# Kernel optimization log

Measured on AMD Instinct MI355X. Metric: run time of the kernel, lower is better.

The kernel has to match this reference:

```python
import jax, jax.numpy as jnp
import numpy as np

LATENT = 128
HIDDEN = 512
N_STEPS = 50
BATCH = 8192


def _linear_init(k, fan_in, fan_out):
    kw, kb = jax.random.split(k)
    lim = 1.0 / np.sqrt(fan_in)
    W = jax.random.uniform(kw, (fan_in, fan_out), minval=-lim, maxval=lim, dtype=jnp.float32)
    b = jax.random.uniform(kb, (fan_out,), minval=-lim, maxval=lim, dtype=jnp.float32)
    return W, b


def setup_inputs() -> dict:
    key = jax.random.key(0)
    ks = jax.random.split(key, 6)
    in_dim = 2 * LATENT + 2  # x + condition + t_emb + target_emb
    W1, b1 = _linear_init(ks[0], in_dim, HIDDEN)
    W2, b2 = _linear_init(ks[1], HIDDEN, HIDDEN)
    W3, b3 = _linear_init(ks[2], HIDDEN, HIDDEN)
    W4, b4 = _linear_init(ks[3], HIDDEN, LATENT)
    condition = jax.random.normal(ks[4], (BATCH, LATENT), dtype=jnp.float32)
    x_init = jax.random.normal(ks[5], (BATCH, LATENT), dtype=jnp.float32)
    return dict(condition=condition, x_init=x_init,
                W1=W1, b1=b1, W2=W2, b2=b2, W3=W3, b3=b3, W4=W4, b4=b4,
                target_survival=1)


def reference(condition, x_init, W1, b1, W2, b2, W3, b3, W4, b4, target_survival):
    n_steps = N_STEPS
    betas = jnp.linspace(1e-4, 0.02, n_steps).astype(x_init.dtype)
    alphas = 1.0 - betas
    alphas_cumprod = jnp.cumprod(alphas)
    batch = condition.shape[0]
    # target = zeros if target_survival else ones (static python scalar)
    target = jnp.full((batch, 1), 0.0 if target_survival else 1.0, dtype=x_init.dtype)
    noise_key = jax.random.key(42)

    def step(x, t):
        t_emb = jnp.full((batch, 1), 1.0, x.dtype) * (t.astype(x.dtype) / n_steps)
        inp = jnp.concatenate([x, condition, t_emb, target], axis=-1)  # [B, 2L+2]
        h = jax.nn.gelu(inp @ W1 + b1, approximate=False)
        h = jax.nn.gelu(h @ W2 + b2, approximate=False)
        h = jax.nn.gelu(h @ W3 + b3, approximate=False)
        noise_pred = h @ W4 + b4  # [B, L]
        noise = jax.random.normal(jax.random.fold_in(noise_key, t), x.shape, x.dtype)
        noise = jnp.where(t > 0, noise, jnp.zeros_like(noise))  # no noise at t=0
        beta_t = betas[t]
        x = (x - beta_t / jnp.sqrt(1.0 - alphas_cumprod[t]) * noise_pred) / jnp.sqrt(alphas[t])
        x = x + jnp.sqrt(beta_t) * noise
        return x, None

    ts = jnp.arange(n_steps - 1, -1, -1)  # reversed(range(n_steps))
    x_final, _ = jax.lax.scan(step, x_init, ts)
    return x_final
```

## Files before the change

### kernel.cpp

```cpp
#include <hip/hip_runtime.h>
#include <stdint.h>
#include <stddef.h>


typedef __bf16 bf16;
typedef __bf16 bf16x4 __attribute__((ext_vector_type(4)));
typedef __bf16 bf16x8 __attribute__((ext_vector_type(8)));
typedef float  floatx4 __attribute__((ext_vector_type(4)));

#define NSTEPS    50
#define WG_ROWS   32
#define XB_STRIDE 136
#define H_STRIDE  520

__device__ __forceinline__ uint32_t rotl32(uint32_t x, int r) {
  return (x << r) | (x >> (32 - r));
}

__device__ __forceinline__ void threefry2x32(uint32_t k0, uint32_t k1,
                                             uint32_t x0, uint32_t x1,
                                             uint32_t& o0, uint32_t& o1) {
  uint32_t k2 = k0 ^ k1 ^ 0x1BD11BDAu;
  x0 += k0; x1 += k1;
#define TF_R(R) { x0 += x1; x1 = rotl32(x1, R); x1 ^= x0; }
  TF_R(13) TF_R(15) TF_R(26) TF_R(6)
  x0 += k1; x1 += k2 + 1u;
  TF_R(17) TF_R(29) TF_R(16) TF_R(24)
  x0 += k2; x1 += k0 + 2u;
  TF_R(13) TF_R(15) TF_R(26) TF_R(6)
  x0 += k0; x1 += k1 + 3u;
  TF_R(17) TF_R(29) TF_R(16) TF_R(24)
  x0 += k1; x1 += k2 + 4u;
  TF_R(13) TF_R(15) TF_R(26) TF_R(6)
  x0 += k2; x1 += k0 + 5u;
#undef TF_R
  o0 = x0; o1 = x1;
}

__device__ __forceinline__ float erfinv_xla(float x) {
  float w = -0.6931471805599453f * __builtin_amdgcn_logf(fmaf(-x, x, 1.0f));
  float p;
  if (w < 5.0f) {
    w -= 2.5f;
    p = 2.81022636e-08f;
    p = fmaf(p, w, 3.43273939e-07f);
    p = fmaf(p, w, -3.5233877e-06f);
    p = fmaf(p, w, -4.39150654e-06f);
    p = fmaf(p, w, 0.00021858087f);
    p = fmaf(p, w, -0.00125372503f);
    p = fmaf(p, w, -0.00417768164f);
    p = fmaf(p, w, 0.246640727f);
    p = fmaf(p, w, 1.50140941f);
  } else {
    w = __builtin_amdgcn_sqrtf(w) - 3.0f;
    p = -0.000200214257f;
    p = fmaf(p, w, 0.000100950558f);
    p = fmaf(p, w, 0.00134934322f);
    p = fmaf(p, w, -0.00367342844f);
    p = fmaf(p, w, 0.00573950773f);
    p = fmaf(p, w, -0.0076224613f);
    p = fmaf(p, w, 0.00943887047f);
    p = fmaf(p, w, 1.00167406f);
    p = fmaf(p, w, 2.83297682f);
  }
  return p * x;
}

__device__ __forceinline__ float gelu_fast(float x) {
  float z  = x * 0.7071067811865475f;
  float az = fabsf(z);
  float t  = __builtin_amdgcn_rcpf(fmaf(0.3275911f, az, 1.0f));
  float p  = fmaf(1.061405429f, t, -1.453152027f);
  p = fmaf(p, t, 1.421413741f);
  p = fmaf(p, t, -0.284496736f);
  p = fmaf(p, t, 0.254829592f);
  p *= t;
  float e  = __builtin_amdgcn_exp2f(az * az * -1.4426950408889634f);
  float er = fmaf(-p, e, 1.0f);
  er = copysignf(er, z);
  return 0.5f * x * (1.0f + er);
}

template<int KSTEPS, int BSTRIDE, int UNROLL>
__device__ __forceinline__ void gemm2t(const bf16* __restrict__ h_lds,
                                       const bf16* __restrict__ A_pk,
                                       int lane, floatx4 (&acc)[2][2]) {
  const int nrow = lane & 15, q = lane >> 4;
  const bf16* b0 = h_lds + nrow * BSTRIDE + q * 8;
  const bf16* a0 = A_pk + lane * 8;
#pragma unroll UNROLL
  for (int ks = 0; ks < KSTEPS; ++ks) {
    bf16x8 bf0 = *(const bf16x8*)(b0 + ks * 32);
    bf16x8 bf1 = *(const bf16x8*)(b0 + 16 * BSTRIDE + ks * 32);
    bf16x8 aA  = *(const bf16x8*)(a0 + ks * 512);
    bf16x8 aB  = *(const bf16x8*)(a0 + (KSTEPS + ks) * 512);
    acc[0][0] = __builtin_amdgcn_mfma_f32_16x16x32_bf16(aA, bf0, acc[0][0], 0, 0, 0);
    acc[0][1] = __builtin_amdgcn_mfma_f32_16x16x32_bf16(aA, bf1, acc[0][1], 0, 0, 0);
    acc[1][0] = __builtin_amdgcn_mfma_f32_16x16x32_bf16(aB, bf0, acc[1][0], 0, 0, 0);
    acc[1][1] = __builtin_amdgcn_mfma_f32_16x16x32_bf16(aB, bf1, acc[1][1], 0, 0, 0);
  }
}

template<int KSTEPS, int BSTRIDE>
__device__ __forceinline__ void gemm1t(const bf16* __restrict__ h_lds,
                                       const bf16* __restrict__ A_pk,
                                       int lane, floatx4& acc) {
  const int nrow = lane & 15, q = lane >> 4;
  const bf16* b0 = h_lds + nrow * BSTRIDE + q * 8;
  const bf16* a0 = A_pk + lane * 8;
#pragma unroll 4
  for (int ks = 0; ks < KSTEPS; ++ks) {
    bf16x8 bfr = *(const bf16x8*)(b0 + ks * 32);
    bf16x8 af  = *(const bf16x8*)(a0 + ks * 512);
    acc = __builtin_amdgcn_mfma_f32_16x16x32_bf16(af, bfr, acc, 0, 0, 0);
  }
}

__global__ void diff_prep(const float* __restrict__ W1, const float* __restrict__ b1,
                          const float* __restrict__ W2, const float* __restrict__ W3,
                          const float* __restrict__ W4, const int* __restrict__ tsurv,
                          bf16* __restrict__ w1p, bf16* __restrict__ w1cp,
                          bf16* __restrict__ w2p, bf16* __restrict__ w3p,
                          bf16* __restrict__ w4p,
                          float* __restrict__ eb1, uint32_t* __restrict__ fk,
                          float* __restrict__ cst) {
  const int tid = blockIdx.x * blockDim.x + threadIdx.x;
  const int nth = gridDim.x * blockDim.x;
  for (int i = tid; i < 512 * 128; i += nth) {
    int j = i & 7, lane = (i >> 3) & 63, ks = (i >> 9) & 3, ntg = i >> 11;
    int n = ntg * 16 + (lane & 15);
    int k = ks * 32 + (lane >> 4) * 8 + j;
    w1p[i]  = (bf16)W1[k * 512 + n];
    w1cp[i] = (bf16)W1[(128 + k) * 512 + n];
  }
  for (int i = tid; i < 512 * 512; i += nth) {
    int j = i & 7, lane = (i >> 3) & 63, ks = (i >> 9) & 15, ntg = i >> 13;
    int n = ntg * 16 + (lane & 15);
    int k = ks * 32 + (lane >> 4) * 8 + j;
    w2p[i] = (bf16)W2[k * 512 + n];
    w3p[i] = (bf16)W3[k * 512 + n];
  }
  for (int i = tid; i < 128 * 512; i += nth) {
    int j = i & 7, lane = (i >> 3) & 63, ks = (i >> 9) & 15, ntg = i >> 13;
    int n = ntg * 16 + (lane & 15);
    int k = ks * 32 + (lane >> 4) * 8 + j;
    w4p[i] = (bf16)W4[k * 128 + n];
  }
  const float tgt = (tsurv[0] != 0) ? 0.0f : 1.0f;
  for (int i = tid; i < NSTEPS * 512; i += nth) {
    int t = i >> 9, n = i & 511;
    eb1[i] = b1[n] + ((float)t / 50.0f) * W1[256 * 512 + n] + tgt * W1[257 * 512 + n];
  }
  if (tid == 0) {
    float ac = 1.0f;
    for (int t = 0; t < NSTEPS; ++t) {
      float beta  = 1e-4f + (0.02f - 1e-4f) * ((float)t / 49.0f);
      float alpha = 1.0f - beta;
      ac *= alpha;
      cst[t]            = beta / sqrtf(1.0f - ac);
      cst[NSTEPS + t]   = 1.0f / sqrtf(alpha);
      cst[2*NSTEPS + t] = sqrtf(beta);
      uint32_t o0, o1;
      threefry2x32(0u, 42u, 0u, (uint32_t)t, o0, o1);
      fk[t] = o0; fk[NSTEPS + t] = o1;
    }
  }
}

__global__ __launch_bounds__(1024, 4) void diff_main(
    const float* __restrict__ cond, const float* __restrict__ xinit,
    const bf16* __restrict__ w1p, const bf16* __restrict__ w1cp,
    const bf16* __restrict__ w2p, const bf16* __restrict__ w3p,
    const bf16* __restrict__ w4p,
    const float* __restrict__ eb1, const float* __restrict__ b2,
    const float* __restrict__ b3, const float* __restrict__ b4,
    const uint32_t* __restrict__ fk, const float* __restrict__ cst,
    float* __restrict__ out) {
  __shared__ bf16 xb[WG_ROWS * XB_STRIDE];
  __shared__ bf16 hbA[WG_ROWS * H_STRIDE];
  __shared__ bf16 hbB[WG_ROWS * H_STRIDE];

  const int tid  = threadIdx.x;
  const int wave = tid >> 6;
  const int lane = tid & 63;
  const int nrow = lane & 15, q = lane >> 4;
  const int r0   = blockIdx.x * WG_ROWS;
  const int mc0  = wave * 32;
  const int qc   = q * 4;

  const int mtile4 = wave & 7;
  const int ntile4 = wave >> 3;
  const int n4     = ntile4 * 16 + nrow;
  const int xc0    = mtile4 * 16 + qc;

  {
    const int row = tid >> 5;
    const int c4  = (tid & 31) * 4;
    float4 a = *(const float4*)(xinit + (size_t)(r0 + row) * 128 + c4);
    float4 c = *(const float4*)(cond  + (size_t)(r0 + row) * 128 + c4);
    bf16x4 x4, c4v;
    x4[0] = (bf16)a.x; x4[1] = (bf16)a.y; x4[2] = (bf16)a.z; x4[3] = (bf16)a.w;
    c4v[0] = (bf16)c.x; c4v[1] = (bf16)c.y; c4v[2] = (bf16)c.z; c4v[3] = (bf16)c.w;
    *(bf16x4*)(xb  + row * XB_STRIDE + c4) = x4;
    *(bf16x4*)(hbA + row * H_STRIDE  + c4) = c4v;
  }
  float4 xreg = *(const float4*)(xinit + (size_t)(r0 + n4) * 128 + xc0);
  __syncthreads();

  floatx4 cpr[2][2] = {};
  gemm2t<4, H_STRIDE, 4>(hbA, w1cp + (wave * 2) * 4 * 512, lane, cpr);
  __syncthreads();

  for (int t = NSTEPS - 1; t >= 0; --t) {
    {
      floatx4 acc[2][2] = {};
      gemm2t<4, XB_STRIDE, 4>(xb, w1p + (wave * 2) * 4 * 512, lane, acc);
      const float* ebt = eb1 + t * 512;
#pragma unroll
      for (int mt = 0; mt < 2; ++mt) {
        const int col = mc0 + mt * 16 + qc;
        float4 bb = *(const float4*)(ebt + col);
#pragma unroll
        for (int nt = 0; nt < 2; ++nt) {
          bf16x4 g;
#pragma unroll
          for (int r = 0; r < 4; ++r)
            g[r] = (bf16)gelu_fast(acc[mt][nt][r] + cpr[mt][nt][r] + ((const float*)&bb)[r]);
          *(bf16x4*)(hbA + (nt * 16 + nrow) * H_STRIDE + col) = g;
        }
      }
    }
    __syncthreads();

    {
      floatx4 acc[2][2] = {};
      gemm2t<16, H_STRIDE, 4>(hbA, w2p + (wave * 2) * 16 * 512, lane, acc);
#pragma unroll
      for (int mt = 0; mt < 2; ++mt) {
        const int col = mc0 + mt * 16 + qc;
        float4 bb = *(const float4*)(b2 + col);
#pragma unroll
        for (int nt = 0; nt < 2; ++nt) {
          bf16x4 g;
#pragma unroll
          for (int r = 0; r < 4; ++r)
            g[r] = (bf16)gelu_fast(acc[mt][nt][r] + ((const float*)&bb)[r]);
          *(bf16x4*)(hbB + (nt * 16 + nrow) * H_STRIDE + col) = g;
        }
      }
    }
    __syncthreads();

    {
      floatx4 acc[2][2] = {};
      gemm2t<16, H_STRIDE, 4>(hbB, w3p + (wave * 2) * 16 * 512, lane, acc);
#pragma unroll
      for (int mt = 0; mt < 2; ++mt) {
        const int col = mc0 + mt * 16 + qc;
        float4 bb = *(const float4*)(b3 + col);
#pragma unroll
        for (int nt = 0; nt < 2; ++nt) {
          bf16x4 g;
#pragma unroll
          for (int r = 0; r < 4; ++r)
            g[r] = (bf16)gelu_fast(acc[mt][nt][r] + ((const float*)&bb)[r]);
          *(bf16x4*)(hbA + (nt * 16 + nrow) * H_STRIDE + col) = g;
        }
      }
    }
    __syncthreads();

    {
      floatx4 acc = {};
      gemm1t<16, H_STRIDE>(hbA + ntile4 * 16 * H_STRIDE,
                           w4p + mtile4 * 16 * 512, lane, acc);
      const float c1 = cst[t], c2 = cst[NSTEPS + t], c3 = cst[2 * NSTEPS + t];
      const uint32_t fk0 = fk[t], fk1 = fk[NSTEPS + t];
      float4 bb = *(const float4*)(b4 + xc0);
      const uint32_t gbase = (uint32_t)(r0 + n4) * 128u + (uint32_t)xc0;
      bf16x4 xpk;
#pragma unroll
      for (int r = 0; r < 4; ++r) {
        float np = acc[r] + ((const float*)&bb)[r];
        float z = 0.0f;
        if (t > 0) {
          uint32_t o0, o1;
          threefry2x32(fk0, fk1, 0u, gbase + (uint32_t)r, o0, o1);
          uint32_t bits = o0 ^ o1;
          float f01 = __uint_as_float((bits >> 9) | 0x3F800000u) - 1.0f;
          float u = f01 * 2.0f + (-0.99999994f);
          u = fmaxf(-0.99999994f, u);
          z = 1.4142135381698608f * erfinv_xla(u);
        }
        float xn = (((float*)&xreg)[r] - c1 * np) * c2 + c3 * z;
        ((float*)&xreg)[r] = xn;
        xpk[r] = (bf16)xn;
      }
      *(bf16x4*)(xb + n4 * XB_STRIDE + xc0) = xpk;
    }
    __syncthreads();
  }

  *(float4*)(out + (size_t)(r0 + n4) * 128 + xc0) = xreg;
}

extern "C" void kernel_launch(void* const* d_in, const int* in_sizes, int n_in,
                              void* d_out, int out_size, void* d_ws, size_t ws_size,
                              hipStream_t stream) {
  const float* cond  = (const float*)d_in[0];
  const float* xinit = (const float*)d_in[1];
  const float* W1 = (const float*)d_in[2];
  const float* b1 = (const float*)d_in[3];
  const float* W2 = (const float*)d_in[4];
  const float* b2 = (const float*)d_in[5];
  const float* W3 = (const float*)d_in[6];
  const float* b3 = (const float*)d_in[7];
  const float* W4 = (const float*)d_in[8];
  const float* b4 = (const float*)d_in[9];
  const int* tsurv = (const int*)d_in[10];

  char* ws = (char*)d_ws;
  bf16* w1p  = (bf16*)(ws + 0);
  bf16* w1cp = (bf16*)(ws + 131072);
  bf16* w2p  = (bf16*)(ws + 262144);
  bf16* w3p  = (bf16*)(ws + 786432);
  bf16* w4p  = (bf16*)(ws + 1310720);
  float* eb1 = (float*)(ws + 1441792);
  uint32_t* fkp = (uint32_t*)(ws + 1544192);
  float* cstp = (float*)(ws + 1544704);

  diff_prep<<<1024, 256, 0, stream>>>(W1, b1, W2, W3, W4, tsurv,
                                      w1p, w1cp, w2p, w3p, w4p, eb1, fkp, cstp);
  diff_main<<<256, 1024, 0, stream>>>(cond, xinit, w1p, w1cp, w2p, w3p, w4p,
                                      eb1, b2, b3, b4, fkp, cstp, (float*)d_out);
}
```

Measured before the change: 995.2 us.

## Keep W1 in registers, prefetch next-layer weights, use lighter barriers

Caches the per-wave W1 fragments in registers for all timesteps, so they are no longer reloaded from global memory at each step. It prefetches the first two k-steps of W2, W3 and W4 fragments before the preceding barrier and epilogue to hide global load latency. It also replaces __syncthreads with an inline s_waitcnt lgkmcnt(0) plus s_barrier, and uses alignbit for the rotates. The extra live registers may reduce occupancy. The custom barrier relies on LDS traffic being the only dependency that needs ordering.

Result: slower. 2.149 ms (+115.9%).

```diff
diff --git a/kernel.cpp b/kernel.cpp
--- a/kernel.cpp
+++ b/kernel.cpp
@@ -13,8 +13,10 @@
 #define XB_STRIDE 136
 #define H_STRIDE  520
 
+#define BAR_LGKM() asm volatile("s_waitcnt lgkmcnt(0)\n\ts_barrier" ::: "memory")
+
 __device__ __forceinline__ uint32_t rotl32(uint32_t x, int r) {
-  return (x << r) | (x >> (32 - r));
+  return __builtin_amdgcn_alignbit(x, x, 32u - (uint32_t)r);
 }
 
 __device__ __forceinline__ void threefry2x32(uint32_t k0, uint32_t k1,
@@ -102,14 +104,54 @@
 }
 
 template<int KSTEPS, int BSTRIDE>
-__device__ __forceinline__ void gemm1t(const bf16* __restrict__ h_lds,
-                                       const bf16* __restrict__ A_pk,
-                                       int lane, floatx4& acc) {
+__device__ __forceinline__ void gemm2t_pre(const bf16* __restrict__ h_lds,
+                                           const bf16* __restrict__ A_pk,
+                                           int lane,
+                                           bf16x8 pA0, bf16x8 pA1,
+                                           bf16x8 pB0, bf16x8 pB1,
+                                           floatx4 (&acc)[2][2]) {
   const int nrow = lane & 15, q = lane >> 4;
   const bf16* b0 = h_lds + nrow * BSTRIDE + q * 8;
   const bf16* a0 = A_pk + lane * 8;
+  {
+    bf16x8 bf0 = *(const bf16x8*)(b0);
+    bf16x8 bf1 = *(const bf16x8*)(b0 + 16 * BSTRIDE);
+    acc[0][0] = __builtin_amdgcn_mfma_f32_16x16x32_bf16(pA0, bf0, acc[0][0], 0, 0, 0);
+    acc[0][1] = __builtin_amdgcn_mfma_f32_16x16x32_bf16(pA0, bf1, acc[0][1], 0, 0, 0);
+    acc[1][0] = __builtin_amdgcn_mfma_f32_16x16x32_bf16(pB0, bf0, acc[1][0], 0, 0, 0);
+    acc[1][1] = __builtin_amdgcn_mfma_f32_16x16x32_bf16(pB0, bf1, acc[1][1], 0, 0, 0);
+    bf0 = *(const bf16x8*)(b0 + 32);
+    bf1 = *(const bf16x8*)(b0 + 16 * BSTRIDE + 32);
+    acc[0][0] = __builtin_amdgcn_mfma_f32_16x16x32_bf16(pA1, bf0, acc[0][0], 0, 0, 0);
+    acc[0][1] = __builtin_amdgcn_mfma_f32_16x16x32_bf16(pA1, bf1, acc[0][1], 0, 0, 0);
+    acc[1][0] = __builtin_amdgcn_mfma_f32_16x16x32_bf16(pB1, bf0, acc[1][0], 0, 0, 0);
+    acc[1][1] = __builtin_amdgcn_mfma_f32_16x16x32_bf16(pB1, bf1, acc[1][1], 0, 0, 0);
+  }
 #pragma unroll 4
-  for (int ks = 0; ks < KSTEPS; ++ks) {
+  for (int ks = 2; ks < KSTEPS; ++ks) {
+    bf16x8 bf0 = *(const bf16x8*)(b0 + ks * 32);
+    bf16x8 bf1 = *(const bf16x8*)(b0 + 16 * BSTRIDE + ks * 32);
+    bf16x8 aA  = *(const bf16x8*)(a0 + ks * 512);
+    bf16x8 aB  = *(const bf16x8*)(a0 + (KSTEPS + ks) * 512);
+    acc[0][0] = __builtin_amdgcn_mfma_f32_16x16x32_bf16(aA, bf0, acc[0][0], 0, 0, 0);
+    acc[0][1] = __builtin_amdgcn_mfma_f32_16x16x32_bf16(aA, bf1, acc[0][1], 0, 0, 0);
+    acc[1][0] = __builtin_amdgcn_mfma_f32_16x16x32_bf16(aB, bf0, acc[1][0], 0, 0, 0);
+    acc[1][1] = __builtin_amdgcn_mfma_f32_16x16x32_bf16(aB, bf1, acc[1][1], 0, 0, 0);
+  }
+}
+
+template<int KSTEPS, int BSTRIDE>
+__device__ __forceinline__ void gemm1t_pre(const bf16* __restrict__ h_lds,
+                                           const bf16* __restrict__ A_pk,
+                                           int lane, bf16x8 p0, bf16x8 p1,
+                                           floatx4& acc) {
+  const int nrow = lane & 15, q = lane >> 4;
+  const bf16* b0 = h_lds + nrow * BSTRIDE + q * 8;
+  const bf16* a0 = A_pk + lane * 8;
+  acc = __builtin_amdgcn_mfma_f32_16x16x32_bf16(p0, *(const bf16x8*)(b0), acc, 0, 0, 0);
+  acc = __builtin_amdgcn_mfma_f32_16x16x32_bf16(p1, *(const bf16x8*)(b0 + 32), acc, 0, 0, 0);
+#pragma unroll 4
+  for (int ks = 2; ks < KSTEPS; ++ks) {
     bf16x8 bfr = *(const bf16x8*)(b0 + ks * 32);
     bf16x8 af  = *(const bf16x8*)(a0 + ks * 512);
     acc = __builtin_amdgcn_mfma_f32_16x16x32_bf16(af, bfr, acc, 0, 0, 0);
@@ -193,6 +235,11 @@
   const int n4     = ntile4 * 16 + nrow;
   const int xc0    = mtile4 * 16 + qc;
 
+  const bf16* w1a = w1p + (wave * 2) * 4 * 512 + lane * 8;
+  const bf16* w2a = w2p + (wave * 2) * 16 * 512 + lane * 8;
+  const bf16* w3a = w3p + (wave * 2) * 16 * 512 + lane * 8;
+  const bf16* w4a = w4p + mtile4 * 16 * 512 + lane * 8;
+
   {
     const int row = tid >> 5;
     const int c4  = (tid & 31) * 4;
@@ -205,16 +252,39 @@
     *(bf16x4*)(hbA + row * H_STRIDE  + c4) = c4v;
   }
   float4 xreg = *(const float4*)(xinit + (size_t)(r0 + n4) * 128 + xc0);
+  const uint32_t gbase = (uint32_t)(r0 + n4) * 128u + (uint32_t)xc0;
+
+  bf16x8 w1r[2][4];
+#pragma unroll
+  for (int mt = 0; mt < 2; ++mt)
+#pragma unroll
+    for (int ks = 0; ks < 4; ++ks)
+      w1r[mt][ks] = *(const bf16x8*)(w1a + (mt * 4 + ks) * 512);
+
   __syncthreads();
 
   floatx4 cpr[2][2] = {};
   gemm2t<4, H_STRIDE, 4>(hbA, w1cp + (wave * 2) * 4 * 512, lane, cpr);
-  __syncthreads();
+  BAR_LGKM();
 
   for (int t = NSTEPS - 1; t >= 0; --t) {
+    bf16x8 p2A0 = *(const bf16x8*)(w2a);
+    bf16x8 p2A1 = *(const bf16x8*)(w2a + 512);
+    bf16x8 p2B0 = *(const bf16x8*)(w2a + 16 * 512);
+    bf16x8 p2B1 = *(const bf16x8*)(w2a + 17 * 512);
+
     {
       floatx4 acc[2][2] = {};
-      gemm2t<4, XB_STRIDE, 4>(xb, w1p + (wave * 2) * 4 * 512, lane, acc);
+      const bf16* b0 = xb + nrow * XB_STRIDE + qc * 2;
+#pragma unroll
+      for (int ks = 0; ks < 4; ++ks) {
+        bf16x8 bf0 = *(const bf16x8*)(b0 + ks * 32);
+        bf16x8 bf1 = *(const bf16x8*)(b0 + 16 * XB_STRIDE + ks * 32);
+        acc[0][0] = __builtin_amdgcn_mfma_f32_16x16x32_bf16(w1r[0][ks], bf0, acc[0][0], 0, 0, 0);
+        acc[0][1] = __builtin_amdgcn_mfma_f32_16x16x32_bf16(w1r[0][ks], bf1, acc[0][1], 0, 0, 0);
+        acc[1][0] = __builtin_amdgcn_mfma_f32_16x16x32_bf16(w1r[1][ks], bf0, acc[1][0], 0, 0, 0);
+        acc[1][1] = __builtin_amdgcn_mfma_f32_16x16x32_bf16(w1r[1][ks], bf1, acc[1][1], 0, 0, 0);
+      }
       const float* ebt = eb1 + t * 512;
 #pragma unroll
       for (int mt = 0; mt < 2; ++mt) {
@@ -230,11 +300,16 @@
         }
       }
     }
-    __syncthreads();
+    BAR_LGKM();
 
     {
       floatx4 acc[2][2] = {};
-      gemm2t<16, H_STRIDE, 4>(hbA, w2p + (wave * 2) * 16 * 512, lane, acc);
+      gemm2t_pre<16, H_STRIDE>(hbA, w2p + (wave * 2) * 16 * 512, lane,
+                               p2A0, p2A1, p2B0, p2B1, acc);
+      bf16x8 p3A0 = *(const bf16x8*)(w3a);
+      bf16x8 p3A1 = *(const bf16x8*)(w3a + 512);
+      bf16x8 p3B0 = *(const bf16x8*)(w3a + 16 * 512);
+      bf16x8 p3B1 = *(const bf16x8*)(w3a + 17 * 512);
 #pragma unroll
       for (int mt = 0; mt < 2; ++mt) {
         const int col = mc0 + mt * 16 + qc;
@@ -248,12 +323,13 @@
           *(bf16x4*)(hbB + (nt * 16 + nrow) * H_STRIDE + col) = g;
         }
       }
-    }
-    __syncthreads();
-
-    {
-      floatx4 acc[2][2] = {};
-      gemm2t<16, H_STRIDE, 4>(hbB, w3p + (wave * 2) * 16 * 512, lane, acc);
+      BAR_LGKM();
+
+      floatx4 acc3[2][2] = {};
+      gemm2t_pre<16, H_STRIDE>(hbB, w3p + (wave * 2) * 16 * 512, lane,
+                               p3A0, p3A1, p3B0, p3B1, acc3);
+      bf16x8 p40 = *(const bf16x8*)(w4a);
+      bf16x8 p41 = *(const bf16x8*)(w4a + 512);
 #pragma unroll
       for (int mt = 0; mt < 2; ++mt) {
         const int col = mc0 + mt * 16 + qc;
@@ -263,25 +339,22 @@
           bf16x4 g;
 #pragma unroll
           for (int r = 0; r < 4; ++r)
-            g[r] = (bf16)gelu_fast(acc[mt][nt][r] + ((const float*)&bb)[r]);
+            g[r] = (bf16)gelu_fast(acc3[mt][nt][r] + ((const float*)&bb)[r]);
           *(bf16x4*)(hbA + (nt * 16 + nrow) * H_STRIDE + col) = g;
         }
       }
-    }
-    __syncthreads();
-
-    {
-      floatx4 acc = {};
-      gemm1t<16, H_STRIDE>(hbA + ntile4 * 16 * H_STRIDE,
-                           w4p + mtile4 * 16 * 512, lane, acc);
+      BAR_LGKM();
+
+      floatx4 acc4 = {};
+      gemm1t_pre<16, H_STRIDE>(hbA + ntile4 * 16 * H_STRIDE, w4p + mtile4 * 16 * 512,
+                               lane, p40, p41, acc4);
       const float c1 = cst[t], c2 = cst[NSTEPS + t], c3 = cst[2 * NSTEPS + t];
       const uint32_t fk0 = fk[t], fk1 = fk[NSTEPS + t];
       float4 bb = *(const float4*)(b4 + xc0);
-      const uint32_t gbase = (uint32_t)(r0 + n4) * 128u + (uint32_t)xc0;
       bf16x4 xpk;
 #pragma unroll
       for (int r = 0; r < 4; ++r) {
-        float np = acc[r] + ((const float*)&bb)[r];
+        float np = acc4[r] + ((const float*)&bb)[r];
         float z = 0.0f;
         if (t > 0) {
           uint32_t o0, o1;
@@ -298,7 +371,7 @@
       }
       *(bf16x4*)(xb + n4 * XB_STRIDE + xc0) = xpk;
     }
-    __syncthreads();
+    BAR_LGKM();
   }
 
   *(float4*)(out + (size_t)(r0 + n4) * 128 + xc0) = xreg;
```
